# Optimization experiments

Hardware: AMD Instinct MI355X
Metric: run time of the kernel (lower is better)

## Reference

```python
import jax, jax.numpy as jnp
import numpy as np

NUM_HEADS = 8
B, S, D = 4, 2048, 512


def setup_inputs() -> dict:
    key = jax.random.key(0)
    ks = jax.random.split(key, 12)
    scale = 1.0 / np.sqrt(D)
    return {
        "v": jax.random.normal(ks[0], (B, S, D), dtype=jnp.float32),
        "k": jax.random.normal(ks[1], (B, S, D), dtype=jnp.float32),
        "q": jax.random.normal(ks[2], (B, S, D), dtype=jnp.float32),
        "Wq": jax.random.normal(ks[3], (D, D), dtype=jnp.float32) * scale,
        "bq": jnp.zeros((D,), dtype=jnp.float32),
        "Wk": jax.random.normal(ks[4], (D, D), dtype=jnp.float32) * scale,
        "bk": jnp.zeros((D,), dtype=jnp.float32),
        "Wv": jax.random.normal(ks[5], (D, D), dtype=jnp.float32) * scale,
        "bv": jnp.zeros((D,), dtype=jnp.float32),
        "Wo": jax.random.normal(ks[6], (D, D), dtype=jnp.float32) * scale,
        "bo": jnp.zeros((D,), dtype=jnp.float32),
        "top_k": 32,
    }


def reference(v, k, q, Wq, bq, Wk, bk, Wv, bv, Wo, bo, top_k):
    dh = D // NUM_HEADS  # per-head depth

    def split_heads(x):  # [B,S,D] -> [B,H,S,dh]
        return x.reshape(B, -1, NUM_HEADS, dh).transpose(0, 2, 1, 3)

    qh = split_heads(q @ Wq + bq)
    kh = split_heads(k @ Wk + bk)
    vh = split_heads(v @ Wv + bv)

    logits = jnp.einsum('bhqd,bhkd->bhqk', qh, kh) / jnp.sqrt(jnp.float32(dh))
    w = jax.nn.softmax(logits, axis=-1)  # [B,H,S,S]

    num_keys = w.shape[-1]
    if top_k < num_keys:
        vals, idx = jax.lax.top_k(w, top_k)  # [B,H,S,top_k]
        bb = jnp.arange(B)[:, None, None, None]
        hh = jnp.arange(NUM_HEADS)[None, :, None, None]
        qq = jnp.arange(S)[None, None, :, None]
        sparse = jnp.zeros_like(w).at[bb, hh, qq, idx].set(vals)
        # tf.linalg.normalize(ord=1): divide by L1 norm along last axis
        w = sparse / jnp.sum(jnp.abs(sparse), axis=-1, keepdims=True)

    attn = jnp.einsum('bhqk,bhkd->bhqd', w, vh)  # [B,H,S,dh]
    concat = attn.transpose(0, 2, 1, 3).reshape(B, -1, D)
    out = concat @ Wo + bo
    return (out, w)
```

## Files before the change

### kernel.cpp

```cpp
#include <hip/hip_runtime.h>
#include <hip/hip_bf16.h>
#include <stdint.h>

#define S_LEN 2048
#define DMODEL 512
#define NH 8
#define DH 64
#define TOPK 32
#define LO_SCALE 4096.0f
#define INV_LO (1.0f/4096.0f)

typedef _Float16 f16;
typedef f16 half8 __attribute__((ext_vector_type(8)));
typedef f16 half4 __attribute__((ext_vector_type(4)));
typedef float floatx4 __attribute__((ext_vector_type(4)));
typedef float f32x4 __attribute__((ext_vector_type(4)));
typedef unsigned long long u64k;

#define AS1 __attribute__((address_space(1)))
#define AS3 __attribute__((address_space(3)))

__device__ __forceinline__ void gl_lds16(const void* g, void* l) {
    __builtin_amdgcn_global_load_lds((const AS1 void*)g, (AS3 void*)l, 16, 0, 0);
}
__device__ __forceinline__ void lds_fence() {
    asm volatile("s_waitcnt lgkmcnt(0)" ::: "memory");
}

__device__ __forceinline__ u64k make_key(float f, int idx) {
    unsigned u = __float_as_uint(f);
    unsigned sv = u ^ ((unsigned)(((int)u) >> 31) | 0x80000000u);
    return ((u64k)sv << 16) | (u64k)(0xFFFFu - (unsigned)idx);
}

__global__ __launch_bounds__(256)
void qkproj(const float* __restrict__ Xq, const float* __restrict__ Xk,
            const float* __restrict__ Wq_, const float* __restrict__ Wk_,
            const float* __restrict__ bq_, const float* __restrict__ bk_,
            float* __restrict__ outQ, float* __restrict__ outK)
{
    __shared__ float As[32][132];
    __shared__ float Bs[32][132];
    const float* X    = blockIdx.z ? Xk  : Xq;
    const float* W    = blockIdx.z ? Wk_ : Wq_;
    const float* bias = blockIdx.z ? bk_ : bq_;
    float* out        = blockIdx.z ? outK : outQ;
    const int tid = threadIdx.x;
    const int tx = tid & 15;
    const int ty = tid >> 4;
    const int m0 = blockIdx.y * 128;
    const int n0 = blockIdx.x * 128;

    float acc[8][8];
#pragma unroll
    for (int i = 0; i < 8; ++i)
#pragma unroll
        for (int j = 0; j < 8; ++j) acc[i][j] = 0.f;

    f32x4 pa[4], pb[4];
#pragma unroll
    for (int u = 0; u < 4; ++u) {
        int id = tid + u * 256;
        pa[u] = *(const f32x4*)(X + (size_t)(m0 + (id >> 3)) * 512 + (id & 7) * 4);
        pb[u] = *(const f32x4*)(W + (size_t)(id >> 5) * 512 + n0 + (id & 31) * 4);
    }

    for (int k0 = 0; k0 < 512; k0 += 32) {
#pragma unroll
        for (int u = 0; u < 4; ++u) {
            int id = tid + u * 256;
            int r = id >> 3, c4 = (id & 7) * 4;
            As[c4 + 0][r] = pa[u].x; As[c4 + 1][r] = pa[u].y;
            As[c4 + 2][r] = pa[u].z; As[c4 + 3][r] = pa[u].w;
            int rb = id >> 5, cb = (id & 31) * 4;
            *(f32x4*)&Bs[rb][cb] = pb[u];
        }
        __syncthreads();
        if (k0 < 480) {
            int kn = k0 + 32;
#pragma unroll
            for (int u = 0; u < 4; ++u) {
                int id = tid + u * 256;
                pa[u] = *(const f32x4*)(X + (size_t)(m0 + (id >> 3)) * 512 + kn + (id & 7) * 4);
                pb[u] = *(const f32x4*)(W + (size_t)(kn + (id >> 5)) * 512 + n0 + (id & 31) * 4);
            }
        }
#pragma unroll 8
        for (int kk = 0; kk < 32; ++kk) {
            float a[8], b[8];
            *(f32x4*)&a[0] = *(const f32x4*)&As[kk][ty * 4];
            *(f32x4*)&a[4] = *(const f32x4*)&As[kk][64 + ty * 4];
            *(f32x4*)&b[0] = *(const f32x4*)&Bs[kk][tx * 4];
            *(f32x4*)&b[4] = *(const f32x4*)&Bs[kk][64 + tx * 4];
#pragma unroll
            for (int i = 0; i < 8; ++i)
#pragma unroll
                for (int j = 0; j < 8; ++j)
                    acc[i][j] = fmaf(a[i], b[j], acc[i][j]);
        }
        __syncthreads();
    }

    float bb[8];
    *(f32x4*)&bb[0] = *(const f32x4*)(bias + n0 + tx * 4);
    *(f32x4*)&bb[4] = *(const f32x4*)(bias + n0 + 64 + tx * 4);

#pragma unroll
    for (int i = 0; i < 8; ++i) {
        int r = m0 + ((i >> 2) << 6) + ty * 4 + (i & 3);
        int b_ = r >> 11, s = r & 2047;
#pragma unroll
        for (int h = 0; h < 2; ++h) {
            int c = n0 + h * 64 + tx * 4;
            f32x4 w = {acc[i][h * 4 + 0] + bb[h * 4 + 0],
                       acc[i][h * 4 + 1] + bb[h * 4 + 1],
                       acc[i][h * 4 + 2] + bb[h * 4 + 2],
                       acc[i][h * 4 + 3] + bb[h * 4 + 3]};
            int hd = c >> 6, d = c & 63;
            float* p = out + (((size_t)(b_ * NH + hd) * S_LEN) + s) * DH + d;
            *(f32x4*)p = w;
        }
    }
}

__global__ __launch_bounds__(256)
void logits_topk(const float* __restrict__ Qh, const float* __restrict__ Kh,
                 float* __restrict__ wbuf)
{
    __shared__ float As[2][32][68];
    __shared__ float Bs[32][132];
    __shared__ u64k  slab[64][32];

    const int tid = threadIdx.x;
    const int lig = tid & 15;
    const int ty  = tid >> 4;
    const int gsh = ((tid & 63) >> 4) << 4;
    const unsigned ltg = (1u << lig) - 1u;
    const int bh = blockIdx.y;
    const int q0 = blockIdx.x * 64;
    const float* Ab = Qh + (size_t)bh * S_LEN * DH;
    const float* Bb = Kh + (size_t)bh * S_LEN * DH;

    auto sort32 = [&](u64k &a0, u64k &a1) {
#pragma unroll
        for (int s = 2; s <= 32; s <<= 1) {
#pragma unroll
            for (int d = s >> 1; d >= 1; d >>= 1) {
                int e0 = 2 * lig;
                if (d == 1) {
                    bool descB = ((e0 & s) == 0);
                    u64k mx = a0 > a1 ? a0 : a1;
                    u64k mn = a0 > a1 ? a1 : a0;
                    a0 = descB ? mx : mn;
                    a1 = descB ? mn : mx;
                } else {
                    bool descB = ((e0 & s) == 0);
                    bool amS   = ((e0 & d) == 0);
                    bool wantMax = (descB == amS);
                    u64k p0 = __shfl_xor(a0, d >> 1, 16);
                    u64k p1 = __shfl_xor(a1, d >> 1, 16);
                    a0 = wantMax ? (a0 > p0 ? a0 : p0) : (a0 > p0 ? p0 : a0);
                    a1 = wantMax ? (a1 > p1 ? a1 : p1) : (a1 > p1 ? p1 : a1);
                }
            }
        }
    };
    auto clean32 = [&](u64k &a0, u64k &a1) {
#pragma unroll
        for (int d = 16; d >= 2; d >>= 1) {
            bool amS = (((2 * lig) & d) == 0);
            u64k p0 = __shfl_xor(a0, d >> 1, 16);
            u64k p1 = __shfl_xor(a1, d >> 1, 16);
            a0 = amS ? (a0 > p0 ? a0 : p0) : (a0 > p0 ? p0 : a0);
            a1 = amS ? (a1 > p1 ? a1 : p1) : (a1 > p1 ? p1 : a1);
        }
        u64k mx = a0 > a1 ? a0 : a1;
        u64k mn = a0 > a1 ? a1 : a0;
        a0 = mx; a1 = mn;
    };

    float acc[4][8];
#pragma unroll
    for (int i = 0; i < 4; ++i)
#pragma unroll
        for (int j = 0; j < 8; ++j) acc[i][j] = 0.f;

    u64k key0[4], key1[4], botk[4];
    int  cnti[4];
#pragma unroll
    for (int i = 0; i < 4; ++i) { key0[i] = 0; key1[i] = 0; botk[i] = 0; cnti[i] = 0; }

#pragma unroll
    for (int u = 0; u < 4; ++u) {
        int id = tid + u * 256;
        int r = id >> 4, c4 = (id & 15) * 4;
        int ch = c4 >> 5, cl = c4 & 31;
        f32x4 x = *(const f32x4*)(Ab + (size_t)(q0 + r) * DH + c4);
        As[ch][cl + 0][r] = x.x * 0.125f;
        As[ch][cl + 1][r] = x.y * 0.125f;
        As[ch][cl + 2][r] = x.z * 0.125f;
        As[ch][cl + 3][r] = x.w * 0.125f;
    }

    f32x4 kb[4];
#pragma unroll
    for (int u = 0; u < 4; ++u) {
        int id = tid + u * 256;
        int r = id >> 3, c4 = (id & 7) * 4;
        kb[u] = *(const f32x4*)(Bb + (size_t)r * DH + c4);
    }

#pragma unroll 1
    for (int kp = 0; kp < 16; ++kp) {
#pragma unroll
        for (int ch = 0; ch < 2; ++ch) {
            __syncthreads();
#pragma unroll
            for (int u = 0; u < 4; ++u) {
                int id = tid + u * 256;
                int r = id >> 3, c4 = (id & 7) * 4;
                Bs[c4 + 0][r] = kb[u].x; Bs[c4 + 1][r] = kb[u].y;
                Bs[c4 + 2][r] = kb[u].z; Bs[c4 + 3][r] = kb[u].w;
            }
            __syncthreads();
            {
                int nkp = ch ? kp + 1 : kp;
                int nch = ch ^ 1;
                if (nkp < 16) {
#pragma unroll
                    for (int u = 0; u < 4; ++u) {
                        int id = tid + u * 256;
                        int r = id >> 3, c4 = (id & 7) * 4;
                        kb[u] = *(const f32x4*)(Bb + (size_t)(nkp * 128 + r) * DH + nch * 32 + c4);
                    }
                }
            }
#pragma unroll 8
            for (int kk = 0; kk < 32; ++kk) {
                float a[4], b[8];
                *(f32x4*)&a[0] = *(const f32x4*)&As[ch][kk][ty * 4];
                *(f32x4*)&b[0] = *(const f32x4*)&Bs[kk][lig * 4];
                *(f32x4*)&b[4] = *(const f32x4*)&Bs[kk][64 + lig * 4];
#pragma unroll
                for (int i = 0; i < 4; ++i)
#pragma unroll
                    for (int j = 0; j < 8; ++j)
                        acc[i][j] = fmaf(a[i], b[j], acc[i][j]);
            }
        }

#pragma unroll
        for (int i = 0; i < 4; ++i) {
            unsigned done = 0;
            if (kp == 0) {
                u64k t0 = 0, t1 = 0; int j0 = 0, j1 = 0;
#pragma unroll
                for (int j = 0; j < 8; ++j) {
                    u64k kj = make_key(acc[i][j], ((j >> 2) << 6) + (lig << 2) + (j & 3));
                    if (kj > t0)      { t1 = t0; j1 = j0; t0 = kj; j0 = j; }
                    else if (kj > t1) { t1 = kj; j1 = j; }
                }
                key0[i] = t0; key1[i] = t1;
                sort32(key0[i], key1[i]);
                botk[i] = __shfl(key1[i], 15, 16);
                cnti[i] = 0;
                done = (1u << j0) | (1u << j1);
            }
            u64k bk = botk[i];
            int c = cnti[i];
#pragma unroll 1
            for (int att = 0; att < 10; ++att) {
                bool ovf = false;
#pragma unroll
                for (int j = 0; j < 8; ++j) {
                    u64k kj = make_key(acc[i][j],
                                       kp * 128 + ((j >> 2) << 6) + (lig << 2) + (j & 3));
                    bool p = (((done >> j) & 1u) == 0u) && (kj > bk);
                    unsigned long long wbm = __ballot(p);
                    unsigned mk = (unsigned)((wbm >> gsh) & 0xFFFFull);
                    if (mk) {
                        int pos = c + __popc(mk & ltg);
                        int tot = c + __popc(mk);
                        if (p && pos < 32) { slab[ty * 4 + i][pos] = kj; done |= 1u << j; }
                        if (tot > 32) { ovf = true; c = 32; } else { c = tot; }
                    }
                }
                if (c > 0 && (ovf || c >= 24 || kp == 15)) {
                    lds_fence();
                    u64k c0 = (2 * lig     < c) ? slab[ty * 4 + i][2 * lig]     : 0ull;
                    u64k c1 = (2 * lig + 1 < c) ? slab[ty * 4 + i][2 * lig + 1] : 0ull;
                    sort32(c0, c1);
                    u64k m0 = __shfl_xor(c1, 15, 16);
                    u64k m1 = __shfl_xor(c0, 15, 16);
                    key0[i] = key0[i] > m0 ? key0[i] : m0;
                    key1[i] = key1[i] > m1 ? key1[i] : m1;
                    clean32(key0[i], key1[i]);
                    bk = __shfl(key1[i], 15, 16);
                    c = 0;
                }
                if (!__any(ovf)) break;
            }
            botk[i] = bk;
            cnti[i] = c;
        }

#pragma unroll
        for (int i = 0; i < 4; ++i)
#pragma unroll
            for (int j = 0; j < 8; ++j) acc[i][j] = 0.f;
    }

#pragma unroll
    for (int i = 0; i < 4; ++i) {
        int r = q0 + ty * 4 + i;
        float* wr = wbuf + ((size_t)bh * S_LEN + r) * S_LEN;
        *(u64k*)(wr + (lig << 2))     = key0[i];
        *(u64k*)(wr + (lig << 2) + 2) = key1[i];
    }
}

__global__ __launch_bounds__(256)
void wsplit2(const float* __restrict__ W0, const float* __restrict__ W1,
             f16* __restrict__ planes)
{
    __shared__ float tile[32][33];
    const float* W = blockIdx.z ? W1 : W0;
    f16* Th = planes + (size_t)blockIdx.z * 524288;
    f16* Tl = Th + 262144;
    const int bx = blockIdx.x * 32;
    const int by = blockIdx.y * 32;
    const int lx = threadIdx.x & 31, ly = threadIdx.x >> 5;
#pragma unroll
    for (int r = ly; r < 32; r += 8)
        tile[r][lx] = W[(size_t)(by + r) * 512 + bx + lx];
    __syncthreads();
#pragma unroll
    for (int r = ly; r < 32; r += 8) {
        float x = tile[lx][r];
        f16 h = (f16)x;
        f16 l = (f16)((x - (float)h) * LO_SCALE);
        Th[(size_t)(bx + r) * 512 + by + lx] = h;
        Tl[(size_t)(bx + r) * 512 + by + lx] = l;
    }
}

__global__ __launch_bounds__(256)
void gemm_x32(const float* __restrict__ X,
              const f16* __restrict__ Bh_, const f16* __restrict__ Bl_,
              const float* __restrict__ bias, float* __restrict__ outF, int mode)
{
    __shared__ f16 sm[16384];
    f16* As_h = sm;       f16* As_l = sm + 4096;
    f16* Bs_h = sm + 8192; f16* Bs_l = sm + 12288;
    const int tid  = threadIdx.x;
    const int lane = tid & 63, wv = tid >> 6;
    const int wm = wv & 1, wn = wv >> 1;
    const int quad = lane >> 4, l15 = lane & 15;
    const int m0 = blockIdx.y * 128, n0 = blockIdx.x * 128;

    floatx4 acc_h[4][4], acc_c[4][4];
    const floatx4 z4 = {0.f, 0.f, 0.f, 0.f};
#pragma unroll
    for (int i = 0; i < 4; ++i)
#pragma unroll
        for (int j = 0; j < 4; ++j) { acc_h[i][j] = z4; acc_c[i][j] = z4; }

    for (int k0 = 0; k0 < 512; k0 += 32) {
        __syncthreads();
#pragma unroll
        for (int c = 0; c < 4; ++c) {
            int r   = c * 32 + (tid >> 3);
            int col = (tid & 7) * 4;
            f32x4 x = *(const f32x4*)(X + (size_t)(m0 + r) * 512 + k0 + col);
            f16 h0 = (f16)x.x, h1 = (f16)x.y, h2 = (f16)x.z, h3 = (f16)x.w;
            half4 hv = {h0, h1, h2, h3};
            half4 lv = {(f16)((x.x - (float)h0) * LO_SCALE),
                        (f16)((x.y - (float)h1) * LO_SCALE),
                        (f16)((x.z - (float)h2) * LO_SCALE),
                        (f16)((x.w - (float)h3) * LO_SCALE)};
            *(half4*)&As_h[r * 32 + col] = hv;
            *(half4*)&As_l[r * 32 + col] = lv;
        }
#pragma unroll
        for (int c = 0; c < 2; ++c) {
            int r    = c * 64 + (wv << 4) + (lane >> 2);
            int ch   = (lane & 3) * 8;
            int lidx = (c * 64 + (wv << 4)) * 32 + lane * 8;
            gl_lds16(Bh_ + (size_t)(n0 + r) * 512 + k0 + ch, &Bs_h[lidx]);
            gl_lds16(Bl_ + (size_t)(n0 + r) * 512 + k0 + ch, &Bs_l[lidx]);
        }
        asm volatile("s_waitcnt vmcnt(0)" ::: "memory");
        __syncthreads();

        half8 bh8[4], bl8[4];
#pragma unroll
        for (int j = 0; j < 4; ++j) {
            int n = wn * 64 + j * 16 + l15;
            bh8[j] = *(const half8*)&Bs_h[n * 32 + quad * 8];
            bl8[j] = *(const half8*)&Bs_l[n * 32 + quad * 8];
        }
#pragma unroll
        for (int i = 0; i < 4; ++i) {
            int m = wm * 64 + i * 16 + l15;
            half8 ah = *(const half8*)&As_h[m * 32 + quad * 8];
            half8 al = *(const half8*)&As_l[m * 32 + quad * 8];
#pragma unroll
            for (int j = 0; j < 4; ++j) {
                acc_h[i][j] = __builtin_amdgcn_mfma_f32_16x16x32_f16(ah, bh8[j], acc_h[i][j], 0, 0, 0);
                acc_c[i][j] = __builtin_amdgcn_mfma_f32_16x16x32_f16(ah, bl8[j], acc_c[i][j], 0, 0, 0);
                acc_c[i][j] = __builtin_amdgcn_mfma_f32_16x16x32_f16(al, bh8[j], acc_c[i][j], 0, 0, 0);
            }
        }
    }

#pragma unroll
    for (int j = 0; j < 4; ++j) {
        int col = n0 + wn * 64 + j * 16 + l15;
        float bv = bias[col];
#pragma unroll
        for (int i = 0; i < 4; ++i) {
            int rbase = m0 + wm * 64 + i * 16 + quad * 4;
#pragma unroll
            for (int rg = 0; rg < 4; ++rg) {
                float r = acc_h[i][j][rg] + acc_c[i][j][rg] * INV_LO + bv;
                int row = rbase + rg;
                if (mode == 2) {
                    outF[(size_t)row * 512 + col] = r;
                } else {
                    int b_ = row >> 11, s = row & 2047, h = col >> 6, d = col & 63;
                    outF[(((size_t)(b_ * NH + h)) * S_LEN + s) * DH + d] = r;
                }
            }
        }
    }
}

__global__ __launch_bounds__(256)
void gemm_x16(const f16* __restrict__ Ah_, const f16* __restrict__ Al_,
              const f16* __restrict__ Bh_, const f16* __restrict__ Bl_,
              const float* __restrict__ bias, float* __restrict__ outF,
              int Ksz, int ldc, int mode)
{
    __shared__ f16 sm[16384];
    f16* As_h = sm;        f16* As_l = sm + 4096;
    f16* Bs_h = sm + 8192; f16* Bs_l = sm + 12288;
    const int tid  = threadIdx.x;
    const int lane = tid & 63, wv = tid >> 6;
    const int wm = wv & 1, wn = wv >> 1;
    const int quad = lane >> 4, l15 = lane & 15;
    const int m0 = blockIdx.y * 128, n0 = blockIdx.x * 128;

    floatx4 acc_h[4][4], acc_c[4][4];
    const floatx4 z4 = {0.f, 0.f, 0.f, 0.f};
#pragma unroll
    for (int i = 0; i < 4; ++i)
#pragma unroll
        for (int j = 0; j < 4; ++j) { acc_h[i][j] = z4; acc_c[i][j] = z4; }

    for (int k0 = 0; k0 < Ksz; k0 += 32) {
        __syncthreads();
#pragma unroll
        for (int c = 0; c < 2; ++c) {
            int r    = c * 64 + (wv << 4) + (lane >> 2);
            int ch   = (lane & 3) * 8;
            int lidx = (c * 64 + (wv << 4)) * 32 + lane * 8;
            gl_lds16(Ah_ + (size_t)(m0 + r) * Ksz + k0 + ch, &As_h[lidx]);
            gl_lds16(Al_ + (size_t)(m0 + r) * Ksz + k0 + ch, &As_l[lidx]);
            gl_lds16(Bh_ + (size_t)(n0 + r) * Ksz + k0 + ch, &Bs_h[lidx]);
            gl_lds16(Bl_ + (size_t)(n0 + r) * Ksz + k0 + ch, &Bs_l[lidx]);
        }
        asm volatile("s_waitcnt vmcnt(0)" ::: "memory");
        __syncthreads();

        half8 bh8[4], bl8[4];
#pragma unroll
        for (int j = 0; j < 4; ++j) {
            int n = wn * 64 + j * 16 + l15;
            bh8[j] = *(const half8*)&Bs_h[n * 32 + quad * 8];
            bl8[j] = *(const half8*)&Bs_l[n * 32 + quad * 8];
        }
#pragma unroll
        for (int i = 0; i < 4; ++i) {
            int m = wm * 64 + i * 16 + l15;
            half8 ah = *(const half8*)&As_h[m * 32 + quad * 8];
            half8 al = *(const half8*)&As_l[m * 32 + quad * 8];
#pragma unroll
            for (int j = 0; j < 4; ++j) {
                acc_h[i][j] = __builtin_amdgcn_mfma_f32_16x16x32_f16(ah, bh8[j], acc_h[i][j], 0, 0, 0);
                acc_c[i][j] = __builtin_amdgcn_mfma_f32_16x16x32_f16(ah, bl8[j], acc_c[i][j], 0, 0, 0);
                acc_c[i][j] = __builtin_amdgcn_mfma_f32_16x16x32_f16(al, bh8[j], acc_c[i][j], 0, 0, 0);
            }
        }
    }

#pragma unroll
    for (int j = 0; j < 4; ++j) {
        int col = n0 + wn * 64 + j * 16 + l15;
        float bv = (mode == 2) ? bias[col] : 0.f;
#pragma unroll
        for (int i = 0; i < 4; ++i) {
            int rbase = m0 + wm * 64 + i * 16 + quad * 4;
#pragma unroll
            for (int rg = 0; rg < 4; ++rg) {
                float r = acc_h[i][j][rg] + acc_c[i][j][rg] * INV_LO;
                int row = rbase + rg;
                outF[(size_t)row * ldc + col] = r + bv;
            }
        }
    }
}

__global__ __launch_bounds__(256)
void topk_scatter(float* __restrict__ wbuf, const float* __restrict__ Vh,
                  f16* __restrict__ attH, f16* __restrict__ attL)
{
    __shared__ float wrow[4][2048];
    __shared__ float win_w[4][TOPK];
    __shared__ int   win_i[4][TOPK];

    const int tid  = threadIdx.x;
    const int wv   = tid >> 6;
    const int lane = tid & 63;
    const int row  = blockIdx.x * 4 + wv;
    float* wr = wbuf + (size_t)row * 2048;

    u64k key = 0;
    if (lane < TOPK) key = ((const u64k*)wr)[lane];
    unsigned sv = (unsigned)(key >> 16);
    unsigned fu = (sv & 0x80000000u) ? (sv ^ 0x80000000u) : ~sv;
    float v = __uint_as_float(fu);
    int idx = (int)(0xFFFFu - (unsigned)(key & 0xFFFFull)) & 2047;

    float m = __shfl(v, 0, 64);
    float e = (lane < TOPK) ? __expf(v - m) : 0.f;

    float mysum = e;
#pragma unroll
    for (int off = 32; off > 0; off >>= 1) mysum += __shfl_xor(mysum, off, 64);
    const float rw = 1.f / mysum;

    if (lane < TOPK) { win_w[wv][lane] = e; win_i[wv][lane] = idx; }

    const f32x4 z = {0.f, 0.f, 0.f, 0.f};
#pragma unroll
    for (int t = 0; t < 8; ++t) ((f32x4*)wrow[wv])[t * 64 + lane] = z;
    lds_fence();
    if (lane < TOPK) wrow[wv][win_i[wv][lane]] = win_w[wv][lane] * rw;
    lds_fence();

#pragma unroll
    for (int t = 0; t < 8; ++t)
        __builtin_nontemporal_store(((f32x4*)wrow[wv])[t * 64 + lane],
                                    (f32x4*)(wr + (size_t)(t * 64 + lane) * 4));

    const int bh = row >> 11;
    const float* Vb = Vh + (size_t)bh * S_LEN * DH;
    float acc = 0.f;
#pragma unroll
    for (int j = 0; j < TOPK; ++j) {
        float wj = win_w[wv][j] * rw;
        int   kj = win_i[wv][j];
        acc = fmaf(wj, Vb[(size_t)kj * DH + lane], acc);
    }
    const int b_ = row >> 14;
    const int h  = (row >> 11) & 7;
    const int s  = row & 2047;
    size_t oidx = (((size_t)b_ * S_LEN) + s) * 512 + h * DH + lane;
    f16 hh = (f16)acc;
    attH[oidx] = hh;
    attL[oidx] = (f16)((acc - (float)hh) * LO_SCALE);
}

extern "C" void kernel_launch(void* const* d_in, const int* in_sizes, int n_in,
                              void* d_out, int out_size, void* d_ws, size_t ws_size,
                              hipStream_t stream) {
    const float* v  = (const float*)d_in[0];
    const float* k  = (const float*)d_in[1];
    const float* q  = (const float*)d_in[2];
    const float* Wq = (const float*)d_in[3];
    const float* bq = (const float*)d_in[4];
    const float* Wk = (const float*)d_in[5];
    const float* bk = (const float*)d_in[6];
    const float* Wv = (const float*)d_in[7];
    const float* bv = (const float*)d_in[8];
    const float* Wo = (const float*)d_in[9];
    const float* bo = (const float*)d_in[10];

    float* out  = (float*)d_out;
    float* wout = out + (size_t)4 * S_LEN * 512;

    char* ws = (char*)d_ws;
    float* Vh   = (float*)ws;
    float* Qh32 = (float*)(ws + 16777216);
    float* Kh32 = (float*)(ws + 33554432);
    f16* WT  = (f16*)(ws + 50331648);
    f16 *WvH = WT,           *WvL = WT + 262144;
    f16 *WoH = WT + 524288,  *WoL = WT + 786432;
    f16* attH = (f16*)(ws + 16777216);
    f16* attL = (f16*)(ws + 25165824);

    wsplit2<<<dim3(16, 16, 2), 256, 0, stream>>>(Wv, Wo, WT);

    qkproj<<<dim3(4, 64, 2), 256, 0, stream>>>(q, k, Wq, Wk, bq, bk, Qh32, Kh32);
    gemm_x32<<<dim3(4, 64), 256, 0, stream>>>(v, WvH, WvL, bv, Vh, 1);

    logits_topk<<<dim3(32, 32), 256, 0, stream>>>(Qh32, Kh32, wout);

    topk_scatter<<<16384, 256, 0, stream>>>(wout, Vh, attH, attL);

    gemm_x16<<<dim3(4, 64, 1), 256, 0, stream>>>(attH, attL, WoH, WoL, bo, out, 512, 512, 2);
}
```

Measured before the change: 1.270 ms.

## Widen logits_topk key tile to 256 and alias B tile with top-k slab

Doubles the key block per outer iteration from 128 to 256, so each thread holds a 4x16 accumulator, and halves the number of outer iterations and top-k merge rounds. The B tile and the candidate slab now share one shared-memory buffer, which keeps LDS use from growing and needs an extra barrier. The candidate carry-over across iterations is removed, so every block now merges its candidates at the end of each iteration. This raises register pressure (64 accumulators plus 8 prefetch vectors) and may lower occupancy.

```diff
diff --git a/kernel.cpp b/kernel.cpp
--- a/kernel.cpp
+++ b/kernel.cpp
@@ -128,8 +128,9 @@
                  float* __restrict__ wbuf)
 {
     __shared__ float As[2][32][68];
-    __shared__ float Bs[32][132];
-    __shared__ u64k  slab[64][32];
+    __shared__ __align__(16) char smemB[33280];
+    float* Bs = (float*)smemB;
+    u64k (*slab)[32] = (u64k(*)[32])smemB;
 
     const int tid = threadIdx.x;
     const int lig = tid & 15;
@@ -179,16 +180,15 @@
         a0 = mx; a1 = mn;
     };
 
-    float acc[4][8];
+    float acc[4][16];
 #pragma unroll
     for (int i = 0; i < 4; ++i)
 #pragma unroll
-        for (int j = 0; j < 8; ++j) acc[i][j] = 0.f;
+        for (int j = 0; j < 16; ++j) acc[i][j] = 0.f;
 
     u64k key0[4], key1[4], botk[4];
-    int  cnti[4];
-#pragma unroll
-    for (int i = 0; i < 4; ++i) { key0[i] = 0; key1[i] = 0; botk[i] = 0; cnti[i] = 0; }
+#pragma unroll
+    for (int i = 0; i < 4; ++i) { key0[i] = 0; key1[i] = 0; botk[i] = 0; }
 
 #pragma unroll
     for (int u = 0; u < 4; ++u) {
@@ -202,52 +202,56 @@
         As[ch][cl + 3][r] = x.w * 0.125f;
     }
 
-    f32x4 kb[4];
-#pragma unroll
-    for (int u = 0; u < 4; ++u) {
+    f32x4 kb[8];
+#pragma unroll
+    for (int u = 0; u < 8; ++u) {
         int id = tid + u * 256;
         int r = id >> 3, c4 = (id & 7) * 4;
         kb[u] = *(const f32x4*)(Bb + (size_t)r * DH + c4);
     }
 
 #pragma unroll 1
-    for (int kp = 0; kp < 16; ++kp) {
+    for (int kp = 0; kp < 8; ++kp) {
 #pragma unroll
         for (int ch = 0; ch < 2; ++ch) {
             __syncthreads();
 #pragma unroll
-            for (int u = 0; u < 4; ++u) {
+            for (int u = 0; u < 8; ++u) {
                 int id = tid + u * 256;
                 int r = id >> 3, c4 = (id & 7) * 4;
-                Bs[c4 + 0][r] = kb[u].x; Bs[c4 + 1][r] = kb[u].y;
-                Bs[c4 + 2][r] = kb[u].z; Bs[c4 + 3][r] = kb[u].w;
+                Bs[(c4 + 0) * 260 + r] = kb[u].x;
+                Bs[(c4 + 1) * 260 + r] = kb[u].y;
+                Bs[(c4 + 2) * 260 + r] = kb[u].z;
+                Bs[(c4 + 3) * 260 + r] = kb[u].w;
             }
             __syncthreads();
             {
                 int nkp = ch ? kp + 1 : kp;
                 int nch = ch ^ 1;
-                if (nkp < 16) {
-#pragma unroll
-                    for (int u = 0; u < 4; ++u) {
+                if (nkp < 8) {
+#pragma unroll
+                    for (int u = 0; u < 8; ++u) {
                         int id = tid + u * 256;
                         int r = id >> 3, c4 = (id & 7) * 4;
-                        kb[u] = *(const f32x4*)(Bb + (size_t)(nkp * 128 + r) * DH + nch * 32 + c4);
+                        kb[u] = *(const f32x4*)(Bb + (size_t)(nkp * 256 + r) * DH + nch * 32 + c4);
                     }
                 }
             }
 #pragma unroll 8
             for (int kk = 0; kk < 32; ++kk) {
-                float a[4], b[8];
+                float a[4], b[16];
                 *(f32x4*)&a[0] = *(const f32x4*)&As[ch][kk][ty * 4];
-                *(f32x4*)&b[0] = *(const f32x4*)&Bs[kk][lig * 4];
-                *(f32x4*)&b[4] = *(const f32x4*)&Bs[kk][64 + lig * 4];
+#pragma unroll
+                for (int h = 0; h < 4; ++h)
+                    *(f32x4*)&b[h * 4] = *(const f32x4*)&Bs[kk * 260 + lig * 4 + h * 64];
 #pragma unroll
                 for (int i = 0; i < 4; ++i)
 #pragma unroll
-                    for (int j = 0; j < 8; ++j)
+                    for (int j = 0; j < 16; ++j)
                         acc[i][j] = fmaf(a[i], b[j], acc[i][j]);
             }
         }
+        __syncthreads();
 
 #pragma unroll
         for (int i = 0; i < 4; ++i) {
@@ -255,7 +259,7 @@
             if (kp == 0) {
                 u64k t0 = 0, t1 = 0; int j0 = 0, j1 = 0;
 #pragma unroll
-                for (int j = 0; j < 8; ++j) {
+                for (int j = 0; j < 16; ++j) {
                     u64k kj = make_key(acc[i][j], ((j >> 2) << 6) + (lig << 2) + (j & 3));
                     if (kj > t0)      { t1 = t0; j1 = j0; t0 = kj; j0 = j; }
                     else if (kj > t1) { t1 = kj; j1 = j; }
@@ -263,18 +267,17 @@
                 key0[i] = t0; key1[i] = t1;
                 sort32(key0[i], key1[i]);
                 botk[i] = __shfl(key1[i], 15, 16);
-                cnti[i] = 0;
                 done = (1u << j0) | (1u << j1);
             }
             u64k bk = botk[i];
-            int c = cnti[i];
+            int c = 0;
 #pragma unroll 1
-            for (int att = 0; att < 10; ++att) {
+            for (int att = 0; att < 12; ++att) {
                 bool ovf = false;
 #pragma unroll
-                for (int j = 0; j < 8; ++j) {
+                for (int j = 0; j < 16; ++j) {
                     u64k kj = make_key(acc[i][j],
-                                       kp * 128 + ((j >> 2) << 6) + (lig << 2) + (j & 3));
+                                       kp * 256 + ((j >> 2) << 6) + (lig << 2) + (j & 3));
                     bool p = (((done >> j) & 1u) == 0u) && (kj > bk);
                     unsigned long long wbm = __ballot(p);
                     unsigned mk = (unsigned)((wbm >> gsh) & 0xFFFFull);
@@ -285,7 +288,8 @@
                         if (tot > 32) { ovf = true; c = 32; } else { c = tot; }
                     }
                 }
-                if (c > 0 && (ovf || c >= 24 || kp == 15)) {
+                bool anyovf = __any(ovf);
+                if (anyovf) {
                     lds_fence();
                     u64k c0 = (2 * lig     < c) ? slab[ty * 4 + i][2 * lig]     : 0ull;
                     u64k c1 = (2 * lig + 1 < c) ? slab[ty * 4 + i][2 * lig + 1] : 0ull;
@@ -297,17 +301,29 @@
                     clean32(key0[i], key1[i]);
                     bk = __shfl(key1[i], 15, 16);
                     c = 0;
+                } else {
+                    break;
                 }
-                if (!__any(ovf)) break;
+            }
+            {
+                lds_fence();
+                u64k c0 = (2 * lig     < c) ? slab[ty * 4 + i][2 * lig]     : 0ull;
+                u64k c1 = (2 * lig + 1 < c) ? slab[ty * 4 + i][2 * lig + 1] : 0ull;
+                sort32(c0, c1);
+                u64k m0 = __shfl_xor(c1, 15, 16);
+                u64k m1 = __shfl_xor(c0, 15, 16);
+                key0[i] = key0[i] > m0 ? key0[i] : m0;
+                key1[i] = key1[i] > m1 ? key1[i] : m1;
+                clean32(key0[i], key1[i]);
+                bk = __shfl(key1[i], 15, 16);
             }
             botk[i] = bk;
-            cnti[i] = c;
         }
 
 #pragma unroll
         for (int i = 0; i < 4; ++i)
 #pragma unroll
-            for (int j = 0; j < 8; ++j) acc[i][j] = 0.f;
+            for (int j = 0; j < 16; ++j) acc[i][j] = 0.f;
     }
 
 #pragma unroll
```

Result: faster. 1.194 ms (-5.9%).
